# Kernel optimization log

Measured on AMD Instinct MI355X. Metric: run time of the kernel, lower is better.

## Reference

```python
import jax, jax.numpy as jnp
import numpy as np

E = 512
H = 8
D = E // H  # head_dim = 64
SCALE = D ** -0.5
NEG_INF = float('-inf')


def layer_norm(x, g, b, eps=1e-5):
    mu = jnp.mean(x, axis=-1, keepdims=True)
    var = jnp.var(x, axis=-1, keepdims=True)
    return (x - mu) * jax.lax.rsqrt(var + eps) * g + b


def setup_inputs() -> dict:
    key = jax.random.key(0)
    ks = jax.random.split(key, 16)
    B, Q, K = 4, 2048, 2048
    inp = {
        'query': jax.random.normal(ks[0], (B, Q, E), jnp.float32),
        'key_value': jax.random.normal(ks[1], (B, K, E), jnp.float32),
        'kv_mask': jax.random.randint(ks[2], (B, K), 0, 2) > 0,
        'sparse_mask': jax.random.randint(ks[3], (B, Q, K), 0, 2) > 0,
        'ln_q_g': jnp.ones((E,), jnp.float32),
        'ln_q_b': jnp.zeros((E,), jnp.float32),
        'ln_kv_g': jnp.ones((E,), jnp.float32),
        'ln_kv_b': jnp.zeros((E,), jnp.float32),
        # Linear weights stored as (in, out): y = x @ W + b
        'Wq': jax.random.normal(ks[4], (E, E), jnp.float32) * (E ** -0.5),
        'bq': jnp.zeros((E,), jnp.float32),
        'Wk': jax.random.normal(ks[5], (E, E), jnp.float32) * (E ** -0.5),
        'bk': jnp.zeros((E,), jnp.float32),
        'Wv': jax.random.normal(ks[6], (E, E), jnp.float32) * (E ** -0.5),
        'bv': jnp.zeros((E,), jnp.float32),
        'Wo': jax.random.normal(ks[7], (E, E), jnp.float32) * (E ** -0.5),
        'bo': jnp.zeros((E,), jnp.float32),
    }
    return inp


def reference(query, key_value, kv_mask, sparse_mask,
              ln_q_g, ln_q_b, ln_kv_g, ln_kv_b,
              Wq, bq, Wk, bk, Wv, bv, Wo, bo):
    B, Qn, _ = query.shape
    Kn = key_value.shape[1]
    qn = layer_norm(query, ln_q_g, ln_q_b)
    kvn = layer_norm(key_value, ln_kv_g, ln_kv_b)
    q = (qn @ Wq + bq).reshape(B, Qn, H, D)
    k = (kvn @ Wk + bk).reshape(B, Kn, H, D)
    v = (kvn @ Wv + bv).reshape(B, Kn, H, D)
    # scores: [B, H, Q, K]
    scores = jnp.einsum('bqhd,bkhd->bhqk', q, k) * SCALE
    mask = kv_mask[:, None, None, :] & sparse_mask[:, None, :, :]
    scores = jnp.where(mask, scores, NEG_INF)
    attn = jax.nn.softmax(scores, axis=-1)
    # nan_to_num(0): rows with no valid key -> all-zero weights
    valid_row = jnp.any(mask, axis=-1, keepdims=True)
    attn = jnp.where(valid_row, attn, 0.0)
    out = jnp.einsum('bhqk,bkhd->bqhd', attn, v).reshape(B, Qn, E)
    return out @ Wo + bo
```

## Files before the change

### kernel.cpp

```cpp
#include <hip/hip_runtime.h>
#include <hip/hip_bf16.h>
#include <math.h>

typedef unsigned short ushort_t;
typedef __attribute__((ext_vector_type(8))) __bf16 bf16x8;
typedef __attribute__((ext_vector_type(4))) float f32x4;
typedef __attribute__((ext_vector_type(16))) float f32x16;
typedef __attribute__((ext_vector_type(4))) unsigned int u32x4;

#define E_DIM 512
#define HEADS 8
#define HD 64
#define SEQ 2048
#define NROWS 8192
#define NEGF (-1e30f)
#define QSCALE 0.18033688011112042f

static __device__ __forceinline__ unsigned short f2b(float f) {
  unsigned int x;
  __builtin_memcpy(&x, &f, 4);
  x += 0x7fffu + ((x >> 16) & 1u);
  return (unsigned short)(x >> 16);
}

static __device__ __forceinline__ unsigned cvt_pk_bf16(float lo, float hi) {
  unsigned r;
  asm("v_cvt_pk_bf16_f32 %0, %1, %2" : "=v"(r) : "v"(lo), "v"(hi));
  return r;
}

static __device__ __forceinline__ int swz(int row, int col) {
  return row * 64 + ((((col >> 3) ^ (row & 7)) & 7) << 3) + (col & 7);
}

static __device__ __forceinline__ void gl2lds16(const ushort_t* g, ushort_t* s) {
#if __has_builtin(__builtin_amdgcn_global_load_lds)
  __builtin_amdgcn_global_load_lds(
      (const __attribute__((address_space(1))) unsigned int*)(uintptr_t)g,
      (__attribute__((address_space(3))) unsigned int*)(uintptr_t)s,
      16, 0, 0);
#else
  int l = threadIdx.x & 63;
  *(u32x4*)(s + l * 8) = *(const u32x4*)g;
#endif
}

__launch_bounds__(256)
__global__ void prep_kernel(const float* __restrict__ Wq, const float* __restrict__ Wk,
                            const float* __restrict__ Wv, const float* __restrict__ Wo,
                            ushort_t* __restrict__ WT,
                            const int* __restrict__ kvm, const int* __restrict__ sp,
                            unsigned long long* __restrict__ bits,
                            const float* __restrict__ xq, const float* __restrict__ xkv,
                            const float* __restrict__ gq, const float* __restrict__ bq,
                            const float* __restrict__ gkv, const float* __restrict__ bkv,
                            ushort_t* __restrict__ yq, ushort_t* __restrict__ ykv) {
  int blk = blockIdx.x;
  int t = threadIdx.x;
  if (blk < 1024) {
    int z = blk >> 8, rem = blk & 255;
    const float* in = (z == 0) ? Wq : (z == 1) ? Wk : (z == 2) ? Wv : Wo;
    ushort_t* o = WT + (size_t)z * E_DIM * E_DIM;
    __shared__ float tile[32 * 33];
    int tx = t & 31, ty = t >> 5;
    int n0 = (rem & 15) * 32, k0 = (rem >> 4) * 32;
#pragma unroll
    for (int i = 0; i < 4; ++i) {
      int k = ty + i * 8;
      tile[k * 33 + tx] = in[(k0 + k) * E_DIM + n0 + tx];
    }
    __syncthreads();
#pragma unroll
    for (int i = 0; i < 4; ++i) {
      int n = ty + i * 8;
      o[(n0 + n) * E_DIM + k0 + tx] = f2b(tile[tx * 33 + n]);
    }
  } else if (blk < 3072) {
    int w = t >> 6, l = t & 63;
    int row = (blk - 1024) * 4 + w;
    int b = row >> 11;
    const int* sprow = sp + ((size_t)row << 11);
    const int* kvrow = kvm + (b << 11);
    unsigned long long* out = bits + ((size_t)row << 5);
#pragma unroll 4
    for (int it = 0; it < 32; ++it) {
      int k = it * 64 + l;
      unsigned long long m = __ballot(sprow[k] != 0 && kvrow[k] != 0);
      if (l == 0) out[it] = m;
    }
  } else {
    int idx = blk - 3072;
    int which = idx >> 11;
    const float* x = which ? xkv : xq;
    const float* g = which ? gkv : gq;
    const float* bb = which ? bkv : bq;
    ushort_t* y = which ? ykv : yq;
    int w = t >> 6, l = t & 63;
    int row = (idx & 2047) * 4 + w;
    f32x4 x0 = *(const f32x4*)&x[row * E_DIM + l * 8];
    f32x4 x1 = *(const f32x4*)&x[row * E_DIM + l * 8 + 4];
    float xf[8], s = 0.f, ss = 0.f;
#pragma unroll
    for (int j = 0; j < 8; ++j) {
      xf[j] = (j < 4) ? x0[j] : x1[j - 4];
      s += xf[j];
      ss += xf[j] * xf[j];
    }
#pragma unroll
    for (int off = 32; off > 0; off >>= 1) {
      s += __shfl_xor(s, off);
      ss += __shfl_xor(ss, off);
    }
    float mu = s * (1.f / 512.f);
    float var = fmaxf(ss * (1.f / 512.f) - mu * mu, 0.f);
    float rs = rsqrtf(var + 1e-5f);
    f32x4 g0 = *(const f32x4*)&g[l * 8];
    f32x4 g1 = *(const f32x4*)&g[l * 8 + 4];
    f32x4 b0 = *(const f32x4*)&bb[l * 8];
    f32x4 b1 = *(const f32x4*)&bb[l * 8 + 4];
#pragma unroll
    for (int j = 0; j < 8; ++j) {
      float gv = (j < 4) ? g0[j] : g1[j - 4];
      float bv = (j < 4) ? b0[j] : b1[j - 4];
      y[row * E_DIM + l * 8 + j] = f2b((xf[j] - mu) * rs * gv + bv);
    }
  }
}

template <int MODE>
static __device__ __forceinline__ void gemm_core128(ushort_t* lA, ushort_t* lB,
                                                    const ushort_t* __restrict__ A,
                                                    const ushort_t* __restrict__ WT,
                                                    const float* __restrict__ bias,
                                                    void* Cv, float scale, int m0, int n0) {
  int t = threadIdx.x, w = t >> 6, l = t & 63;
  int quad = l >> 4, l15 = l & 15;
  int wm_ = w >> 1, wn_ = w & 1;
  int csrc = ((l & 7) ^ (l >> 3)) * 8;
  int rln = l >> 3;

  f32x4 acc[4][4] = {};
  for (int kk = 0; kk < E_DIM; kk += 64) {
    __syncthreads();
#pragma unroll
    for (int i = 0; i < 4; ++i) {
      int r0 = i * 32 + w * 8;
      gl2lds16(&A[(size_t)(m0 + r0 + rln) * E_DIM + kk + csrc], &lA[r0 * 64]);
      gl2lds16(&WT[(size_t)(n0 + r0 + rln) * E_DIM + kk + csrc], &lB[r0 * 64]);
    }
    __syncthreads();
#pragma unroll
    for (int ks = 0; ks < 2; ++ks) {
      bf16x8 af[4], bf[4];
#pragma unroll
      for (int mt = 0; mt < 4; ++mt)
        af[mt] = *(const bf16x8*)&lA[swz(wm_ * 64 + mt * 16 + l15, ks * 32 + quad * 8)];
#pragma unroll
      for (int nt = 0; nt < 4; ++nt)
        bf[nt] = *(const bf16x8*)&lB[swz(wn_ * 64 + nt * 16 + l15, ks * 32 + quad * 8)];
#pragma unroll
      for (int mt = 0; mt < 4; ++mt)
#pragma unroll
        for (int nt = 0; nt < 4; ++nt)
          acc[mt][nt] = __builtin_amdgcn_mfma_f32_16x16x32_bf16(af[mt], bf[nt], acc[mt][nt], 0, 0, 0);
    }
  }

#pragma unroll
  for (int nt = 0; nt < 4; ++nt) {
    int col = n0 + wn_ * 64 + nt * 16 + l15;
    float bv = bias[col];
    if constexpr (MODE == 2) {
      int h = col >> 6, d = col & 63;
#pragma unroll
      for (int mt = 0; mt < 4; ++mt) {
        int row = m0 + wm_ * 64 + mt * 16 + quad * 4;
        int b = row >> 11, k = row & 2047;
        union { ushort_t u[4]; uint2 v; } pk;
#pragma unroll
        for (int r = 0; r < 4; ++r) pk.u[r] = f2b(acc[mt][nt][r] + bv);
        *(uint2*)&((ushort_t*)Cv)[((((size_t)(b * HEADS + h)) * HD + d) << 11) + k] = pk.v;
      }
    } else {
#pragma unroll
      for (int mt = 0; mt < 4; ++mt) {
#pragma unroll
        for (int r = 0; r < 4; ++r) {
          int rowm = m0 + wm_ * 64 + mt * 16 + quad * 4 + r;
          float val = (acc[mt][nt][r] + bv) * scale;
          if constexpr (MODE == 0)
            ((ushort_t*)Cv)[rowm * E_DIM + col] = f2b(val);
          else
            ((float*)Cv)[rowm * E_DIM + col] = val;
        }
      }
    }
  }
}

__launch_bounds__(256)
__global__ void gemm128_bf16(const ushort_t* __restrict__ A, const ushort_t* __restrict__ WT,
                             const float* __restrict__ bias, ushort_t* __restrict__ C, float scale) {
  __shared__ ushort_t lA[128 * 64];
  __shared__ ushort_t lB[128 * 64];
  gemm_core128<0>(lA, lB, A, WT, bias, C, scale, blockIdx.x * 128, blockIdx.y * 128);
}

__launch_bounds__(256)
__global__ void gemm128_f32(const ushort_t* __restrict__ A, const ushort_t* __restrict__ WT,
                            const float* __restrict__ bias, float* __restrict__ C) {
  __shared__ ushort_t lA[128 * 64];
  __shared__ ushort_t lB[128 * 64];
  gemm_core128<1>(lA, lB, A, WT, bias, C, 1.f, blockIdx.x * 128, blockIdx.y * 128);
}

__launch_bounds__(256)
__global__ void proj2_kernel(const ushort_t* __restrict__ qn, const ushort_t* __restrict__ WTq,
                             const float* __restrict__ bq, ushort_t* __restrict__ qp,
                             const ushort_t* __restrict__ kvn, const ushort_t* __restrict__ WTv,
                             const float* __restrict__ bv, ushort_t* __restrict__ Vt) {
  __shared__ ushort_t lA[128 * 64];
  __shared__ ushort_t lB[128 * 64];
  int m0 = blockIdx.x * 128, n0 = blockIdx.y * 128;
  if (blockIdx.z == 0) gemm_core128<0>(lA, lB, qn, WTq, bq, qp, QSCALE, m0, n0);
  else                 gemm_core128<2>(lA, lB, kvn, WTv, bv, Vt, 1.f, m0, n0);
}

__launch_bounds__(256)
__global__ void attn_kernel(const ushort_t* __restrict__ Qp, const ushort_t* __restrict__ Kp,
                            const ushort_t* __restrict__ Vt,
                            const unsigned long long* __restrict__ bits,
                            ushort_t* __restrict__ ctx) {
  __shared__ ushort_t sQ[128 * 64];
  __shared__ ushort_t sK[2][64 * 64];
  __shared__ ushort_t sV[2][64 * 64];
  int t = threadIdx.x, w = t >> 6, l = t & 63;
  int l31 = l & 31, half = l >> 5;
  int q0 = blockIdx.x * 128;
  int h = blockIdx.y;
  int b = blockIdx.z;
  int bh = b * HEADS + h;
  int myq = w * 32 + l31;
  int csrc = ((l & 7) ^ (l >> 3)) * 8;
  int rln = l >> 3;

#pragma unroll
  for (int it = 0; it < 4; ++it) {
    int r0 = it * 32 + w * 8;
    gl2lds16(&Qp[(size_t)(b * SEQ + q0 + r0 + rln) * E_DIM + h * HD + csrc], &sQ[r0 * 64]);
  }
#pragma unroll
  for (int it = 0; it < 2; ++it) {
    int r0 = it * 32 + w * 8;
    gl2lds16(&Kp[(size_t)(b * SEQ + r0 + rln) * E_DIM + h * HD + csrc], &sK[0][r0 * 64]);
    gl2lds16(&Vt[((size_t)bh * HD + r0 + rln) * SEQ + csrc], &sV[0][r0 * 64]);
  }
  __syncthreads();

  bf16x8 qf[4];
#pragma unroll
  for (int ds = 0; ds < 4; ++ds)
    qf[ds] = *(const bf16x8*)&sQ[swz(myq, ds * 16 + 8 * half)];

  const unsigned long long* mrow = bits + ((size_t)(b * SEQ + q0 + myq) << 5);
  float ls0 = 0.f, ls1 = 0.f, ls2 = 0.f, ls3 = 0.f;
  f32x16 o0 = {}, o1 = {};
  int cur = 0;

  for (int kt = 0; kt < 32; ++kt) {
    unsigned long long wmask = mrow[kt];

    if (kt < 31) {
      int k0 = (kt + 1) * 64;
      int nxt = cur ^ 1;
#pragma unroll
      for (int it = 0; it < 2; ++it) {
        int r0 = it * 32 + w * 8;
        gl2lds16(&Kp[(size_t)(b * SEQ + k0 + r0 + rln) * E_DIM + h * HD + csrc], &sK[nxt][r0 * 64]);
        gl2lds16(&Vt[((size_t)bh * HD + r0 + rln) * SEQ + k0 + csrc], &sV[nxt][r0 * 64]);
      }
    }

    f32x16 s0 = {}, s1 = {};
    __builtin_amdgcn_s_setprio(1);
#pragma unroll
    for (int ds = 0; ds < 4; ++ds) {
      bf16x8 kf0 = *(const bf16x8*)&sK[cur][swz(l31, ds * 16 + 8 * half)];
      bf16x8 kf1 = *(const bf16x8*)&sK[cur][swz(32 + l31, ds * 16 + 8 * half)];
      s0 = __builtin_amdgcn_mfma_f32_32x32x16_bf16(kf0, qf[ds], s0, 0, 0, 0);
      s1 = __builtin_amdgcn_mfma_f32_32x32x16_bf16(kf1, qf[ds], s1, 0, 0, 0);
    }
    __builtin_amdgcn_s_setprio(0);

    bf16x8 pf[4];
#pragma unroll
    for (int kt2 = 0; kt2 < 2; ++kt2) {
      const f32x16& sv = kt2 ? s1 : s0;
      unsigned h32 = ((unsigned)(wmask >> (32 * kt2))) >> (4 * half);
      unsigned wa[4], wb[4];
#pragma unroll
      for (int g = 0; g < 4; ++g) {
        unsigned gb = h32 >> (8 * g);
        float p0 = exp2f((gb & 1u)        ? sv[g * 4 + 0] : NEGF);
        float p1 = exp2f(((gb >> 1) & 1u) ? sv[g * 4 + 1] : NEGF);
        float p2 = exp2f(((gb >> 2) & 1u) ? sv[g * 4 + 2] : NEGF);
        float p3 = exp2f(((gb >> 3) & 1u) ? sv[g * 4 + 3] : NEGF);
        ls0 += p0; ls1 += p1; ls2 += p2; ls3 += p3;
        wa[g] = cvt_pk_bf16(p0, p1);
        wb[g] = cvt_pk_bf16(p2, p3);
      }
      asm("v_permlane32_swap_b32 %0, %1" : "+v"(wa[0]), "+v"(wa[1]));
      asm("v_permlane32_swap_b32 %0, %1" : "+v"(wb[0]), "+v"(wb[1]));
      asm("v_permlane32_swap_b32 %0, %1" : "+v"(wa[2]), "+v"(wa[3]));
      asm("v_permlane32_swap_b32 %0, %1" : "+v"(wb[2]), "+v"(wb[3]));
      union { unsigned u[4]; bf16x8 v; } f0, f1;
      f0.u[0] = wa[0]; f0.u[1] = wb[0]; f0.u[2] = wa[1]; f0.u[3] = wb[1];
      f1.u[0] = wa[2]; f1.u[1] = wb[2]; f1.u[2] = wa[3]; f1.u[3] = wb[3];
      pf[kt2 * 2 + 0] = f0.v;
      pf[kt2 * 2 + 1] = f1.v;
    }

    __builtin_amdgcn_s_setprio(1);
#pragma unroll
    for (int ksp = 0; ksp < 4; ++ksp) {
      bf16x8 vf0 = *(const bf16x8*)&sV[cur][swz(l31, ksp * 16 + 8 * half)];
      bf16x8 vf1 = *(const bf16x8*)&sV[cur][swz(32 + l31, ksp * 16 + 8 * half)];
      o0 = __builtin_amdgcn_mfma_f32_32x32x16_bf16(vf0, pf[ksp], o0, 0, 0, 0);
      o1 = __builtin_amdgcn_mfma_f32_32x32x16_bf16(vf1, pf[ksp], o1, 0, 0, 0);
    }
    __builtin_amdgcn_s_setprio(0);

    __syncthreads();
    cur ^= 1;
  }

  float lsum = (ls0 + ls1) + (ls2 + ls3);
  lsum += __shfl_xor(lsum, 32);
  float inv = (lsum > 0.f) ? 1.f / lsum : 0.f;
  size_t base = (size_t)(b * SEQ + q0 + myq) * E_DIM + h * HD;
#pragma unroll
  for (int dt = 0; dt < 2; ++dt) {
    const f32x16& oo = dt ? o1 : o0;
#pragma unroll
    for (int g = 0; g < 4; ++g) {
      union { ushort_t u[4]; uint2 v; } ov;
#pragma unroll
      for (int r = 0; r < 4; ++r) ov.u[r] = f2b(oo[g * 4 + r] * inv);
      *(uint2*)&ctx[base + dt * 32 + g * 8 + 4 * half] = ov.v;
    }
  }
}

extern "C" void kernel_launch(void* const* d_in, const int* in_sizes, int n_in,
                              void* d_out, int out_size, void* d_ws, size_t ws_size,
                              hipStream_t stream) {
  const float* query     = (const float*)d_in[0];
  const float* key_value = (const float*)d_in[1];
  const int*   kv_mask   = (const int*)d_in[2];
  const int*   sp_mask   = (const int*)d_in[3];
  const float* ln_q_g  = (const float*)d_in[4];
  const float* ln_q_b  = (const float*)d_in[5];
  const float* ln_kv_g = (const float*)d_in[6];
  const float* ln_kv_b = (const float*)d_in[7];
  const float* Wq = (const float*)d_in[8];
  const float* bq = (const float*)d_in[9];
  const float* Wk = (const float*)d_in[10];
  const float* bk = (const float*)d_in[11];
  const float* Wv = (const float*)d_in[12];
  const float* bv = (const float*)d_in[13];
  const float* Wo = (const float*)d_in[14];
  const float* bo = (const float*)d_in[15];

  const size_t NB = (size_t)NROWS * E_DIM;
  char* ws = (char*)d_ws;
  ushort_t* bufA = (ushort_t*)ws;
  ushort_t* bufB = bufA + NB;
  ushort_t* WT   = bufB + NB;
  ushort_t* WTq = WT;
  ushort_t* WTk = WTq + E_DIM * E_DIM;
  ushort_t* WTv = WTk + E_DIM * E_DIM;
  ushort_t* WTo = WTv + E_DIM * E_DIM;
  unsigned long long* bits = (unsigned long long*)(WTo + E_DIM * E_DIM);

  ushort_t* dlo = (ushort_t*)d_out;
  ushort_t* dhi = dlo + NB;

  prep_kernel<<<7168, 256, 0, stream>>>(Wq, Wk, Wv, Wo, WT, kv_mask, sp_mask, bits,
                                        query, key_value, ln_q_g, ln_q_b, ln_kv_g, ln_kv_b,
                                        dlo, bufA);

  proj2_kernel<<<dim3(64, 4, 2), 256, 0, stream>>>(dlo, WTq, bq, dhi,
                                                   bufA, WTv, bv, bufB);

  gemm128_bf16<<<dim3(64, 4), 256, 0, stream>>>(bufA, WTk, bk, dlo, 1.f);

  attn_kernel<<<dim3(16, HEADS, 4), 256, 0, stream>>>(dhi, dlo, bufB, bits, bufA);

  gemm128_f32<<<dim3(64, 4), 256, 0, stream>>>(bufA, WTo, bo, (float*)d_out);
}
```

Before: 287.4 us.

## Split attention key range across warp pairs with LDS merge and remapped grid

```diff
diff --git a/kernel.cpp b/kernel.cpp
--- a/kernel.cpp
+++ b/kernel.cpp
@@ -26,6 +26,12 @@
 static __device__ __forceinline__ unsigned cvt_pk_bf16(float lo, float hi) {
   unsigned r;
   asm("v_cvt_pk_bf16_f32 %0, %1, %2" : "=v"(r) : "v"(lo), "v"(hi));
+  return r;
+}
+
+static __device__ __forceinline__ float fexp2(float x) {
+  float r;
+  asm("v_exp_f32 %0, %1" : "=v"(r) : "v"(x));
   return r;
 }
 
@@ -231,62 +237,60 @@
                             const ushort_t* __restrict__ Vt,
                             const unsigned long long* __restrict__ bits,
                             ushort_t* __restrict__ ctx) {
-  __shared__ ushort_t sQ[128 * 64];
-  __shared__ ushort_t sK[2][64 * 64];
-  __shared__ ushort_t sV[2][64 * 64];
+  __shared__ __align__(16) char smemb[40960];
+  ushort_t* sQ = (ushort_t*)smemb;
   int t = threadIdx.x, w = t >> 6, l = t & 63;
+  int qw = w & 1, ks = w >> 1;
+  ushort_t* sK = (ushort_t*)(smemb + 8192 + ks * 8192);
+  ushort_t* sV = (ushort_t*)(smemb + 24576 + ks * 8192);
   int l31 = l & 31, half = l >> 5;
-  int q0 = blockIdx.x * 128;
-  int h = blockIdx.y;
-  int b = blockIdx.z;
+
+  int flat = blockIdx.x;
+  int work = (flat & 7) * 128 + (flat >> 3);
+  int qblk = work & 31;
+  int h = (work >> 5) & 7;
+  int b = work >> 8;
+  int q0 = qblk * 64;
   int bh = b * HEADS + h;
-  int myq = w * 32 + l31;
+  int myq = qw * 32 + l31;
   int csrc = ((l & 7) ^ (l >> 3)) * 8;
   int rln = l >> 3;
 
 #pragma unroll
-  for (int it = 0; it < 4; ++it) {
-    int r0 = it * 32 + w * 8;
+  for (int it = 0; it < 2; ++it) {
+    int r0 = w * 16 + it * 8;
     gl2lds16(&Qp[(size_t)(b * SEQ + q0 + r0 + rln) * E_DIM + h * HD + csrc], &sQ[r0 * 64]);
   }
-#pragma unroll
-  for (int it = 0; it < 2; ++it) {
-    int r0 = it * 32 + w * 8;
-    gl2lds16(&Kp[(size_t)(b * SEQ + r0 + rln) * E_DIM + h * HD + csrc], &sK[0][r0 * 64]);
-    gl2lds16(&Vt[((size_t)bh * HD + r0 + rln) * SEQ + csrc], &sV[0][r0 * 64]);
-  }
-  __syncthreads();
-
-  bf16x8 qf[4];
-#pragma unroll
-  for (int ds = 0; ds < 4; ++ds)
-    qf[ds] = *(const bf16x8*)&sQ[swz(myq, ds * 16 + 8 * half)];
 
   const unsigned long long* mrow = bits + ((size_t)(b * SEQ + q0 + myq) << 5);
   float ls0 = 0.f, ls1 = 0.f, ls2 = 0.f, ls3 = 0.f;
   f32x16 o0 = {}, o1 = {};
-  int cur = 0;
-
-  for (int kt = 0; kt < 32; ++kt) {
+  bf16x8 qf[4];
+
+  for (int t16 = 0; t16 < 16; ++t16) {
+    int kt = t16 * 2 + ks;
+    int k0 = kt * 64;
     unsigned long long wmask = mrow[kt];
-
-    if (kt < 31) {
-      int k0 = (kt + 1) * 64;
-      int nxt = cur ^ 1;
-#pragma unroll
-      for (int it = 0; it < 2; ++it) {
-        int r0 = it * 32 + w * 8;
-        gl2lds16(&Kp[(size_t)(b * SEQ + k0 + r0 + rln) * E_DIM + h * HD + csrc], &sK[nxt][r0 * 64]);
-        gl2lds16(&Vt[((size_t)bh * HD + r0 + rln) * SEQ + k0 + csrc], &sV[nxt][r0 * 64]);
-      }
+    __syncthreads();
+#pragma unroll
+    for (int it = 0; it < 4; ++it) {
+      int r0 = (it * 2 + qw) * 8;
+      gl2lds16(&Kp[(size_t)(b * SEQ + k0 + r0 + rln) * E_DIM + h * HD + csrc], &sK[r0 * 64]);
+      gl2lds16(&Vt[((size_t)bh * HD + r0 + rln) * SEQ + k0 + csrc], &sV[r0 * 64]);
+    }
+    __syncthreads();
+    if (t16 == 0) {
+#pragma unroll
+      for (int ds = 0; ds < 4; ++ds)
+        qf[ds] = *(const bf16x8*)&sQ[swz(myq, ds * 16 + 8 * half)];
     }
 
     f32x16 s0 = {}, s1 = {};
     __builtin_amdgcn_s_setprio(1);
 #pragma unroll
     for (int ds = 0; ds < 4; ++ds) {
-      bf16x8 kf0 = *(const bf16x8*)&sK[cur][swz(l31, ds * 16 + 8 * half)];
-      bf16x8 kf1 = *(const bf16x8*)&sK[cur][swz(32 + l31, ds * 16 + 8 * half)];
+      bf16x8 kf0 = *(const bf16x8*)&sK[swz(l31, ds * 16 + 8 * half)];
+      bf16x8 kf1 = *(const bf16x8*)&sK[swz(32 + l31, ds * 16 + 8 * half)];
       s0 = __builtin_amdgcn_mfma_f32_32x32x16_bf16(kf0, qf[ds], s0, 0, 0, 0);
       s1 = __builtin_amdgcn_mfma_f32_32x32x16_bf16(kf1, qf[ds], s1, 0, 0, 0);
     }
@@ -301,10 +305,10 @@
 #pragma unroll
       for (int g = 0; g < 4; ++g) {
         unsigned gb = h32 >> (8 * g);
-        float p0 = exp2f((gb & 1u)        ? sv[g * 4 + 0] : NEGF);
-        float p1 = exp2f(((gb >> 1) & 1u) ? sv[g * 4 + 1] : NEGF);
-        float p2 = exp2f(((gb >> 2) & 1u) ? sv[g * 4 + 2] : NEGF);
-        float p3 = exp2f(((gb >> 3) & 1u) ? sv[g * 4 + 3] : NEGF);
+        float p0 = fexp2((gb & 1u)        ? sv[g * 4 + 0] : NEGF);
+        float p1 = fexp2(((gb >> 1) & 1u) ? sv[g * 4 + 1] : NEGF);
+        float p2 = fexp2(((gb >> 2) & 1u) ? sv[g * 4 + 2] : NEGF);
+        float p3 = fexp2(((gb >> 3) & 1u) ? sv[g * 4 + 3] : NEGF);
         ls0 += p0; ls1 += p1; ls2 += p2; ls3 += p3;
         wa[g] = cvt_pk_bf16(p0, p1);
         wb[g] = cvt_pk_bf16(p2, p3);
@@ -323,30 +327,47 @@
     __builtin_amdgcn_s_setprio(1);
 #pragma unroll
     for (int ksp = 0; ksp < 4; ++ksp) {
-      bf16x8 vf0 = *(const bf16x8*)&sV[cur][swz(l31, ksp * 16 + 8 * half)];
-      bf16x8 vf1 = *(const bf16x8*)&sV[cur][swz(32 + l31, ksp * 16 + 8 * half)];
+      bf16x8 vf0 = *(const bf16x8*)&sV[swz(l31, ksp * 16 + 8 * half)];
+      bf16x8 vf1 = *(const bf16x8*)&sV[swz(32 + l31, ksp * 16 + 8 * half)];
       o0 = __builtin_amdgcn_mfma_f32_32x32x16_bf16(vf0, pf[ksp], o0, 0, 0, 0);
       o1 = __builtin_amdgcn_mfma_f32_32x32x16_bf16(vf1, pf[ksp], o1, 0, 0, 0);
     }
     __builtin_amdgcn_s_setprio(0);
-
-    __syncthreads();
-    cur ^= 1;
   }
 
   float lsum = (ls0 + ls1) + (ls2 + ls3);
   lsum += __shfl_xor(lsum, 32);
-  float inv = (lsum > 0.f) ? 1.f / lsum : 0.f;
-  size_t base = (size_t)(b * SEQ + q0 + myq) * E_DIM + h * HD;
-#pragma unroll
-  for (int dt = 0; dt < 2; ++dt) {
-    const f32x16& oo = dt ? o1 : o0;
-#pragma unroll
-    for (int g = 0; g < 4; ++g) {
-      union { ushort_t u[4]; uint2 v; } ov;
-#pragma unroll
-      for (int r = 0; r < 4; ++r) ov.u[r] = f2b(oo[g * 4 + r] * inv);
-      *(uint2*)&ctx[base + dt * 32 + g * 8 + 4 * half] = ov.v;
+
+  __syncthreads();
+  float* mrg = (float*)(smemb + 8192);
+  if (ks == 1) {
+    float* e = mrg + (qw * 64 + l) * 33;
+#pragma unroll
+    for (int r = 0; r < 16; ++r) e[r] = o0[r];
+#pragma unroll
+    for (int r = 0; r < 16; ++r) e[16 + r] = o1[r];
+    e[32] = lsum;
+  }
+  __syncthreads();
+  if (ks == 0) {
+    const float* e = mrg + (qw * 64 + l) * 33;
+#pragma unroll
+    for (int r = 0; r < 16; ++r) o0[r] += e[r];
+#pragma unroll
+    for (int r = 0; r < 16; ++r) o1[r] += e[16 + r];
+    lsum += e[32];
+    float inv = (lsum > 0.f) ? 1.f / lsum : 0.f;
+    size_t base = (size_t)(b * SEQ + q0 + myq) * E_DIM + h * HD;
+#pragma unroll
+    for (int dt = 0; dt < 2; ++dt) {
+      const f32x16& oo = dt ? o1 : o0;
+#pragma unroll
+      for (int g = 0; g < 4; ++g) {
+        union { ushort_t u[4]; uint2 v; } ov;
+#pragma unroll
+        for (int r = 0; r < 4; ++r) ov.u[r] = f2b(oo[g * 4 + r] * inv);
+        *(uint2*)&ctx[base + dt * 32 + g * 8 + 4 * half] = ov.v;
+      }
     }
   }
 }
@@ -394,7 +415,7 @@
 
   gemm128_bf16<<<dim3(64, 4), 256, 0, stream>>>(bufA, WTk, bk, dlo, 1.f);
 
-  attn_kernel<<<dim3(16, HEADS, 4), 256, 0, stream>>>(dhi, dlo, bufB, bits, bufA);
+  attn_kernel<<<1024, 256, 0, stream>>>(dhi, dlo, bufB, bits, bufA);
 
   gemm128_f32<<<dim3(64, 4), 256, 0, stream>>>(bufA, WTo, bo, (float*)d_out);
 }
```

Result: faster. 269.6 us (-6.2%).
